# Performance work log

Hardware: AMD Instinct MI355X
Metric: run time of the kernel (lower is better)

## Reference

```python
import jax, jax.numpy as jnp
import numpy as np

B, T, D, F, E = 8, 2048, 1024, 4096, 16
C_FACTOR = 1.25
LB_W = 0.01


def setup_inputs() -> dict:
    key = jax.random.key(0)
    ks = jax.random.split(key, 4)
    x = jax.random.normal(ks[0], (B, T, D), dtype=jnp.float32)
    Wr = jax.random.normal(ks[1], (E, D), dtype=jnp.float32) * 0.02
    W1 = jax.random.normal(ks[2], (E, F, D), dtype=jnp.float32) * 0.02
    b1 = jnp.zeros((E, F), dtype=jnp.float32)
    W2 = jax.random.normal(ks[3], (E, D, F), dtype=jnp.float32) * 0.02
    b2 = jnp.zeros((E, D), dtype=jnp.float32)
    return {"x": x, "Wr": Wr, "W1": W1, "b1": b1, "W2": W2, "b2": b2}


def reference(x, Wr, W1, b1, W2, b2):
    Bs, Ts, Ds = x.shape
    Es = Wr.shape[0]
    tokens = Bs * Ts
    xf = x.reshape(tokens, Ds)

    # router
    logits = xf @ Wr.T                       # [tokens, E]
    probs = jax.nn.softmax(logits, axis=-1)
    top1 = jnp.argmax(probs, axis=-1)        # [tokens]
    top1p = jnp.max(probs, axis=-1)          # [tokens]

    capacity = int(C_FACTOR * tokens / Es)   # static python int

    onehot = jax.nn.one_hot(top1, Es, dtype=jnp.int32)        # [tokens, E]
    f = onehot.sum(axis=0).astype(probs.dtype) / tokens
    p = probs.mean(axis=0)
    lb_loss = Es * jnp.sum(f * p) * LB_W

    # faithful reproduction of idx[::expert_capacity]: among tokens routed to
    # expert e (in token order), keep only those whose rank % capacity == 0
    ranks = jnp.cumsum(onehot, axis=0) - 1                     # [tokens, E]
    keep = (onehot == 1) & (ranks % capacity == 0)             # [tokens, E]
    K = (tokens - 1) // capacity + 1                           # static max kept per expert

    idx = jax.vmap(lambda m: jnp.nonzero(m, size=K, fill_value=0)[0])(keep.T)  # [E, K]
    valid = jnp.take_along_axis(keep.T, idx, axis=1)           # [E, K] bool

    xg = xf[idx]                                               # [E, K, D]
    h = jax.nn.gelu(jnp.einsum('ekd,efd->ekf', xg, W1) + b1[:, None, :], approximate=False)
    eo = jnp.einsum('ekf,edf->ekd', h, W2) + b2[:, None, :]    # [E, K, D]
    scale = top1p[idx] * valid.astype(eo.dtype)                # [E, K]
    eo = eo * scale[..., None]

    out = jnp.zeros_like(xf).at[idx.reshape(-1)].add(eo.reshape(-1, Ds))
    return out.reshape(Bs, Ts, Ds), lb_loss
```

## Files before the change

kernel.cpp:

```cpp
#include <hip/hip_runtime.h>
#include <math.h>


#define TOKENS 16384
#define DD     1024
#define FF     4096
#define EE     16
#define CAP    1280
#define KMAX   13
#define NBLK   256

__global__ __launch_bounds__(256) void router_kernel(
    const float* __restrict__ x, const float* __restrict__ Wr,
    int* __restrict__ top1, float* __restrict__ top1p,
    int* __restrict__ blockhist, float* __restrict__ blockpsum)
{
    __shared__ float wrj[EE * 256];
    __shared__ float p_acc[EE];
    __shared__ int   hist[EE];

    const int tid  = threadIdx.x;
    const int wave = tid >> 6;
    const int lane = tid & 63;
    const int blk  = blockIdx.x;

    if (tid < EE) { p_acc[tid] = 0.0f; hist[tid] = 0; }

    for (int it = 0; it < 4; ++it) {
        const int tbase = blk * 64 + wave * 16 + it * 4;

        float4 xr[4][4];
        #pragma unroll
        for (int t = 0; t < 4; ++t) {
            const float4* xp = (const float4*)(x + (size_t)(tbase + t) * DD);
            #pragma unroll
            for (int j = 0; j < 4; ++j) xr[t][j] = xp[j * 64 + lane];
        }

        float acc[4][EE];
        #pragma unroll
        for (int t = 0; t < 4; ++t)
            #pragma unroll
            for (int e = 0; e < EE; ++e) acc[t][e] = 0.0f;

        for (int j = 0; j < 4; ++j) {
            __syncthreads();
            #pragma unroll
            for (int k = 0; k < 4; ++k) {
                int i = tid + k * 256;
                int e = i >> 6, c = i & 63;
                ((float4*)wrj)[i] = ((const float4*)Wr)[e * 256 + j * 64 + c];
            }
            __syncthreads();
            #pragma unroll
            for (int e = 0; e < EE; ++e) {
                float4 w = ((const float4*)(wrj + e * 256))[lane];
                #pragma unroll
                for (int t = 0; t < 4; ++t) {
                    acc[t][e] += xr[t][j].x * w.x + xr[t][j].y * w.y
                               + xr[t][j].z * w.z + xr[t][j].w * w.w;
                }
            }
        }

        #pragma unroll
        for (int t = 0; t < 4; ++t)
            #pragma unroll
            for (int e = 0; e < EE; ++e) {
                float v = acc[t][e];
                v += __shfl_xor(v, 32);
                v += __shfl_xor(v, 16);
                v += __shfl_xor(v, 8);
                v += __shfl_xor(v, 4);
                v += __shfl_xor(v, 2);
                v += __shfl_xor(v, 1);
                acc[t][e] = v;
            }

        if (lane < 4) {
            float lg[EE];
            #pragma unroll
            for (int e = 0; e < EE; ++e) {
                float v = acc[3][e];
                if (lane == 2) v = acc[2][e];
                if (lane == 1) v = acc[1][e];
                if (lane == 0) v = acc[0][e];
                lg[e] = v;
            }
            const int gt = tbase + lane;
            float mx = lg[0]; int bi = 0;
            #pragma unroll
            for (int e = 1; e < EE; ++e)
                if (lg[e] > mx) { mx = lg[e]; bi = e; }
            float pr[EE];
            float s = 0.0f;
            #pragma unroll
            for (int e = 0; e < EE; ++e) { pr[e] = expf(lg[e] - mx); s += pr[e]; }
            const float inv = 1.0f / s;
            top1[gt]  = bi;
            top1p[gt] = inv;
            #pragma unroll
            for (int e = 0; e < EE; ++e) atomicAdd(&p_acc[e], pr[e] * inv);
            atomicAdd(&hist[bi], 1);
        }
    }
    __syncthreads();
    if (tid < EE) {
        blockhist[blk * EE + tid] = hist[tid];
        blockpsum[blk * EE + tid] = p_acc[tid];
    }
}

__global__ __launch_bounds__(256) void scan_kernel(
    const int* __restrict__ blockhist, const float* __restrict__ blockpsum,
    int* __restrict__ base, int* __restrict__ nkept,
    const int* __restrict__ top1, float* __restrict__ mult0,
    float* __restrict__ lb_out)
{
    __shared__ int   hist_l[NBLK * EE];
    __shared__ int   gsum[EE * 16];
    __shared__ float fps[EE * 16];
    __shared__ float fp[EE];
    __shared__ int   nk_l[EE];

    const int tid = threadIdx.x;
    for (int i = tid; i < NBLK * EE; i += 256) hist_l[i] = blockhist[i];
    __syncthreads();

    const int e = tid >> 4, g = tid & 15;
    int s = 0;
    float sp = 0.0f;
    for (int b = g * 16; b < g * 16 + 16; ++b) {
        s  += hist_l[b * EE + e];
        sp += blockpsum[b * EE + e];
    }
    gsum[e * 16 + g] = s;
    fps[e * 16 + g]  = sp;
    __syncthreads();

    int pre = 0;
    for (int g2 = 0; g2 < g; ++g2) pre += gsum[e * 16 + g2];
    int run = pre;
    for (int b = g * 16; b < g * 16 + 16; ++b) {
        base[b * EE + e] = run;
        run += hist_l[b * EE + e];
    }
    if (g == 15) {
        const int c = run;
        const int nk = (c > 0) ? ((c - 1) / CAP + 1) : 0;
        nkept[e] = nk;
        nk_l[e]  = nk;
        float ps = 0.0f;
        for (int g2 = 0; g2 < 16; ++g2) ps += fps[e * 16 + g2];
        fp[e] = ((float)c / (float)TOKENS) * (ps / (float)TOKENS);
    }
    __syncthreads();
    if (tid == 0) {
        const int e0 = top1[0];
        mult0[0] = (float)(1 + KMAX - nk_l[e0]);
        float sum = 0.0f;
        for (int i = 0; i < EE; ++i) sum += fp[i];
        lb_out[0] = (float)EE * sum * 0.01f;
    }
}

__global__ __launch_bounds__(64) void keep_kernel(
    const int* __restrict__ top1, const float* __restrict__ top1p,
    const int* __restrict__ base, const float* __restrict__ mult0,
    int* __restrict__ kept_tok, float* __restrict__ kept_scale,
    int* __restrict__ slotmap)
{
    __shared__ int t1[64];
    const int tid = threadIdx.x;
    const int blk = blockIdx.x;
    const int gt  = blk * 64 + tid;
    const int e   = top1[gt];
    t1[tid] = e;
    __syncthreads();
    int r = 0;
    for (int i = 0; i < tid; ++i) r += (t1[i] == e) ? 1 : 0;
    const int rank = base[blk * EE + e] + r;
    int sm = -1;
    if (rank % CAP == 0) {
        const int slot = rank / CAP;
        sm = e * KMAX + slot;
        kept_tok[sm] = gt;
        float sc = top1p[gt];
        if (gt == 0) sc *= mult0[0];
        kept_scale[sm] = sc;
    }
    slotmap[gt] = sm;
}

__global__ __launch_bounds__(256) void expert1_kernel(
    const float* __restrict__ x, const float* __restrict__ W1,
    const float* __restrict__ b1, const int* __restrict__ nkept,
    const int* __restrict__ kept_tok, float* __restrict__ h)
{
    const int e    = blockIdx.x >> 8;
    const int fblk = blockIdx.x & 255;
    const int ne   = nkept[e];
    if (ne == 0) return;
    const int wave = threadIdx.x >> 6;
    const int lane = threadIdx.x & 63;

    for (int s = 0; s < ne; ++s) {
        const int t = kept_tok[e * KMAX + s];
        const float4* xp = (const float4*)(x + (size_t)t * DD);
        #pragma unroll
        for (int i = 0; i < 4; ++i) {
            const int f = fblk * 16 + wave * 4 + i;
            const float4* wrow = (const float4*)(W1 + ((size_t)e * FF + f) * DD);
            float d = 0.0f;
            #pragma unroll
            for (int k = 0; k < 4; ++k) {
                const float4 w  = wrow[k * 64 + lane];
                const float4 xv = xp[k * 64 + lane];
                d += w.x*xv.x + w.y*xv.y + w.z*xv.z + w.w*xv.w;
            }
            d += __shfl_xor(d, 32);
            d += __shfl_xor(d, 16);
            d += __shfl_xor(d, 8);
            d += __shfl_xor(d, 4);
            d += __shfl_xor(d, 2);
            d += __shfl_xor(d, 1);
            if (lane == 0) {
                const float v = d + b1[e * FF + f];
                h[((size_t)e * KMAX + s) * FF + f] =
                    0.5f * v * (1.0f + erff(v * 0.70710678118654752440f));
            }
        }
    }
}

__global__ __launch_bounds__(256) void expert2_kernel(
    const float* __restrict__ h, const float* __restrict__ W2,
    const float* __restrict__ b2, const int* __restrict__ nkept,
    const float* __restrict__ kept_scale, float* __restrict__ eo)
{
    const int e    = blockIdx.x >> 8;
    const int dblk = blockIdx.x & 255;
    const int ne   = nkept[e];
    if (ne == 0) return;
    const int wave = threadIdx.x >> 6;
    const int lane = threadIdx.x & 63;
    const int d    = dblk * 4 + wave;

    const float4* wrow = (const float4*)(W2 + ((size_t)e * DD + d) * FF);
    for (int s = 0; s < ne; ++s) {
        const float4* hp = (const float4*)(h + ((size_t)e * KMAX + s) * FF);
        float acc = 0.0f;
        #pragma unroll
        for (int k = 0; k < 16; ++k) {
            const float4 w  = wrow[k * 64 + lane];
            const float4 hv = hp[k * 64 + lane];
            acc += w.x*hv.x + w.y*hv.y + w.z*hv.z + w.w*hv.w;
        }
        acc += __shfl_xor(acc, 32);
        acc += __shfl_xor(acc, 16);
        acc += __shfl_xor(acc, 8);
        acc += __shfl_xor(acc, 4);
        acc += __shfl_xor(acc, 2);
        acc += __shfl_xor(acc, 1);
        if (lane == 0) {
            const float sc = kept_scale[e * KMAX + s];
            eo[((size_t)e * KMAX + s) * DD + d] = sc * (acc + b2[e * DD + d]);
        }
    }
}

__global__ __launch_bounds__(256) void expand_kernel(
    const float* __restrict__ eo, const int* __restrict__ slotmap,
    float* __restrict__ out)
{
    const int nf4 = TOKENS * DD / 4;
    int idx = blockIdx.x * 256 + threadIdx.x;
    const int stride = 4096 * 256;
    for (; idx < nf4; idx += stride) {
        const int t    = idx >> 8;
        const int slot = slotmap[t];
        float4 v = make_float4(0.0f, 0.0f, 0.0f, 0.0f);
        if (slot >= 0) v = ((const float4*)eo)[slot * 256 + (idx & 255)];
        ((float4*)out)[idx] = v;
    }
}

extern "C" void kernel_launch(void* const* d_in, const int* in_sizes, int n_in,
                              void* d_out, int out_size, void* d_ws, size_t ws_size,
                              hipStream_t stream) {
    const float* x  = (const float*)d_in[0];
    const float* Wr = (const float*)d_in[1];
    const float* W1 = (const float*)d_in[2];
    const float* b1 = (const float*)d_in[3];
    const float* W2 = (const float*)d_in[4];
    const float* b2 = (const float*)d_in[5];
    float* out = (float*)d_out;

    char* p = (char*)d_ws;
    int*   top1       = (int*)p;    p += (size_t)TOKENS * 4;
    float* top1p      = (float*)p;  p += (size_t)TOKENS * 4;
    int*   slotmap    = (int*)p;    p += (size_t)TOKENS * 4;
    int*   blockhist  = (int*)p;    p += (size_t)NBLK * EE * 4;
    float* blockpsum  = (float*)p;  p += (size_t)NBLK * EE * 4;
    int*   base       = (int*)p;    p += (size_t)NBLK * EE * 4;
    int*   nkept      = (int*)p;    p += 256;
    float* mult0      = (float*)p;  p += 256;
    int*   kept_tok   = (int*)p;    p += 1024;
    float* kept_scale = (float*)p;  p += 1024;
    float* eo         = (float*)p;  p += (size_t)EE * KMAX * DD * 4;
    float* h          = (float*)p;  p += (size_t)EE * KMAX * FF * 4;
    (void)ws_size; (void)in_sizes; (void)n_in;

    router_kernel<<<NBLK, 256, 0, stream>>>(x, Wr, top1, top1p,
                                            blockhist, blockpsum);
    scan_kernel<<<1, 256, 0, stream>>>(blockhist, blockpsum, base, nkept,
                                       top1, mult0, out + (size_t)out_size - 1);
    keep_kernel<<<NBLK, 64, 0, stream>>>(top1, top1p, base, mult0,
                                         kept_tok, kept_scale, slotmap);
    expert1_kernel<<<EE * 256, 256, 0, stream>>>(x, W1, b1, nkept, kept_tok, h);
    expert2_kernel<<<EE * 256, 256, 0, stream>>>(h, W2, b2, nkept, kept_scale, eo);
    expand_kernel<<<4096, 256, 0, stream>>>(eo, slotmap, out);
}
```

Measured before the change: 667.9 us.

## Retile router, expert GEMV, and scan kernels for more parallelism and reuse

The router now uses twice as many blocks, each covering 32 tokens, and reads Wr straight from global/L1 instead of staging it through LDS with barriers. The scan and keep kernels change to match the 32-token histogram granularity. expert1 issues all W1 and x loads up front and writes h as a float4. expert2 caches the h row in LDS and computes two output rows per wave. Together these aim to raise memory-level parallelism and cut sync overhead, at the cost of more registers and a finer-grained scan.

```diff
diff --git a/kernel.cpp b/kernel.cpp
--- a/kernel.cpp
+++ b/kernel.cpp
@@ -8,14 +8,13 @@
 #define EE     16
 #define CAP    1280
 #define KMAX   13
-#define NBLK   256
+#define NBLK   512
 
 __global__ __launch_bounds__(256) void router_kernel(
     const float* __restrict__ x, const float* __restrict__ Wr,
     int* __restrict__ top1, float* __restrict__ top1p,
     int* __restrict__ blockhist, float* __restrict__ blockpsum)
 {
-    __shared__ float wrj[EE * 256];
     __shared__ float p_acc[EE];
     __shared__ int   hist[EE];
 
@@ -25,17 +24,15 @@
     const int blk  = blockIdx.x;
 
     if (tid < EE) { p_acc[tid] = 0.0f; hist[tid] = 0; }
-
-    for (int it = 0; it < 4; ++it) {
-        const int tbase = blk * 64 + wave * 16 + it * 4;
-
-        float4 xr[4][4];
-        #pragma unroll
-        for (int t = 0; t < 4; ++t) {
-            const float4* xp = (const float4*)(x + (size_t)(tbase + t) * DD);
-            #pragma unroll
-            for (int j = 0; j < 4; ++j) xr[t][j] = xp[j * 64 + lane];
-        }
+    __syncthreads();
+
+    const float4* Wr4 = (const float4*)Wr;
+    for (int it = 0; it < 2; ++it) {
+        const int tbase = blk * 32 + wave * 8 + it * 4;
+        const float4* xp0 = (const float4*)(x + (size_t)(tbase + 0) * DD);
+        const float4* xp1 = (const float4*)(x + (size_t)(tbase + 1) * DD);
+        const float4* xp2 = (const float4*)(x + (size_t)(tbase + 2) * DD);
+        const float4* xp3 = (const float4*)(x + (size_t)(tbase + 3) * DD);
 
         float acc[4][EE];
         #pragma unroll
@@ -43,23 +40,19 @@
             #pragma unroll
             for (int e = 0; e < EE; ++e) acc[t][e] = 0.0f;
 
+        #pragma unroll
         for (int j = 0; j < 4; ++j) {
-            __syncthreads();
-            #pragma unroll
-            for (int k = 0; k < 4; ++k) {
-                int i = tid + k * 256;
-                int e = i >> 6, c = i & 63;
-                ((float4*)wrj)[i] = ((const float4*)Wr)[e * 256 + j * 64 + c];
-            }
-            __syncthreads();
+            const float4 x0 = xp0[j * 64 + lane];
+            const float4 x1 = xp1[j * 64 + lane];
+            const float4 x2 = xp2[j * 64 + lane];
+            const float4 x3 = xp3[j * 64 + lane];
             #pragma unroll
             for (int e = 0; e < EE; ++e) {
-                float4 w = ((const float4*)(wrj + e * 256))[lane];
-                #pragma unroll
-                for (int t = 0; t < 4; ++t) {
-                    acc[t][e] += xr[t][j].x * w.x + xr[t][j].y * w.y
-                               + xr[t][j].z * w.z + xr[t][j].w * w.w;
-                }
+                const float4 w = Wr4[e * 256 + j * 64 + lane];
+                acc[0][e] += x0.x*w.x + x0.y*w.y + x0.z*w.z + x0.w*w.w;
+                acc[1][e] += x1.x*w.x + x1.y*w.y + x1.z*w.z + x1.w*w.w;
+                acc[2][e] += x2.x*w.x + x2.y*w.y + x2.z*w.z + x2.w*w.w;
+                acc[3][e] += x3.x*w.x + x3.y*w.y + x3.z*w.z + x3.w*w.w;
             }
         }
 
@@ -130,7 +123,7 @@
     const int e = tid >> 4, g = tid & 15;
     int s = 0;
     float sp = 0.0f;
-    for (int b = g * 16; b < g * 16 + 16; ++b) {
+    for (int b = g * 32; b < g * 32 + 32; ++b) {
         s  += hist_l[b * EE + e];
         sp += blockpsum[b * EE + e];
     }
@@ -141,7 +134,7 @@
     int pre = 0;
     for (int g2 = 0; g2 < g; ++g2) pre += gsum[e * 16 + g2];
     int run = pre;
-    for (int b = g * 16; b < g * 16 + 16; ++b) {
+    for (int b = g * 32; b < g * 32 + 32; ++b) {
         base[b * EE + e] = run;
         run += hist_l[b * EE + e];
     }
@@ -177,9 +170,11 @@
     const int e   = top1[gt];
     t1[tid] = e;
     __syncthreads();
+    const int start = tid & 32;
     int r = 0;
-    for (int i = 0; i < tid; ++i) r += (t1[i] == e) ? 1 : 0;
-    const int rank = base[blk * EE + e] + r;
+    for (int i = start; i < tid; ++i) r += (t1[i] == e) ? 1 : 0;
+    const int hb   = gt >> 5;
+    const int rank = base[hb * EE + e] + r;
     int sm = -1;
     if (rank % CAP == 0) {
         const int slot = rank / CAP;
@@ -203,32 +198,61 @@
     if (ne == 0) return;
     const int wave = threadIdx.x >> 6;
     const int lane = threadIdx.x & 63;
+    const int f0   = fblk * 16 + wave * 4;
+    const float4* wr0 = (const float4*)(W1 + ((size_t)e * FF + f0) * DD);
 
     for (int s = 0; s < ne; ++s) {
         const int t = kept_tok[e * KMAX + s];
         const float4* xp = (const float4*)(x + (size_t)t * DD);
+        float4 xv[4];
+        #pragma unroll
+        for (int k = 0; k < 4; ++k) xv[k] = xp[k * 64 + lane];
+
+        float4 wv[4][4];
+        #pragma unroll
+        for (int i = 0; i < 4; ++i)
+            #pragma unroll
+            for (int k = 0; k < 4; ++k)
+                wv[i][k] = wr0[i * 256 + k * 64 + lane];
+
+        float d[4];
         #pragma unroll
         for (int i = 0; i < 4; ++i) {
-            const int f = fblk * 16 + wave * 4 + i;
-            const float4* wrow = (const float4*)(W1 + ((size_t)e * FF + f) * DD);
-            float d = 0.0f;
+            float acc = 0.0f;
             #pragma unroll
             for (int k = 0; k < 4; ++k) {
-                const float4 w  = wrow[k * 64 + lane];
-                const float4 xv = xp[k * 64 + lane];
-                d += w.x*xv.x + w.y*xv.y + w.z*xv.z + w.w*xv.w;
-            }
-            d += __shfl_xor(d, 32);
-            d += __shfl_xor(d, 16);
-            d += __shfl_xor(d, 8);
-            d += __shfl_xor(d, 4);
-            d += __shfl_xor(d, 2);
-            d += __shfl_xor(d, 1);
-            if (lane == 0) {
-                const float v = d + b1[e * FF + f];
-                h[((size_t)e * KMAX + s) * FF + f] =
-                    0.5f * v * (1.0f + erff(v * 0.70710678118654752440f));
-            }
+                acc += wv[i][k].x * xv[k].x + wv[i][k].y * xv[k].y
+                     + wv[i][k].z * xv[k].z + wv[i][k].w * xv[k].w;
+            }
+            d[i] = acc;
+        }
+
+        #pragma unroll
+        for (int off = 32; off >= 1; off >>= 1) {
+            #pragma unroll
+            for (int i = 0; i < 4; ++i) d[i] += __shfl_xor(d[i], off);
+        }
+
+        if (lane == 0) {
+            const float* bp = b1 + e * FF + f0;
+            float4 hv;
+            {
+                const float v = d[0] + bp[0];
+                hv.x = 0.5f * v * (1.0f + erff(v * 0.70710678118654752440f));
+            }
+            {
+                const float v = d[1] + bp[1];
+                hv.y = 0.5f * v * (1.0f + erff(v * 0.70710678118654752440f));
+            }
+            {
+                const float v = d[2] + bp[2];
+                hv.z = 0.5f * v * (1.0f + erff(v * 0.70710678118654752440f));
+            }
+            {
+                const float v = d[3] + bp[3];
+                hv.w = 0.5f * v * (1.0f + erff(v * 0.70710678118654752440f));
+            }
+            *(float4*)(h + ((size_t)e * KMAX + s) * FF + f0) = hv;
         }
     }
 }
@@ -238,33 +262,44 @@
     const float* __restrict__ b2, const int* __restrict__ nkept,
     const float* __restrict__ kept_scale, float* __restrict__ eo)
 {
-    const int e    = blockIdx.x >> 8;
-    const int dblk = blockIdx.x & 255;
+    __shared__ float hs[FF];
+    const int e    = blockIdx.x >> 7;
+    const int dblk = blockIdx.x & 127;
     const int ne   = nkept[e];
     if (ne == 0) return;
-    const int wave = threadIdx.x >> 6;
-    const int lane = threadIdx.x & 63;
-    const int d    = dblk * 4 + wave;
-
-    const float4* wrow = (const float4*)(W2 + ((size_t)e * DD + d) * FF);
+    const int tid  = threadIdx.x;
+    const int wave = tid >> 6;
+    const int lane = tid & 63;
+    const int d0   = dblk * 8 + wave * 2;
+
+    const float4* wr0 = (const float4*)(W2 + ((size_t)e * DD + d0) * FF);
     for (int s = 0; s < ne; ++s) {
+        __syncthreads();
         const float4* hp = (const float4*)(h + ((size_t)e * KMAX + s) * FF);
-        float acc = 0.0f;
+        #pragma unroll
+        for (int q = 0; q < 4; ++q)
+            ((float4*)hs)[q * 256 + tid] = hp[q * 256 + tid];
+        __syncthreads();
+
+        float a0 = 0.0f, a1 = 0.0f;
         #pragma unroll
         for (int k = 0; k < 16; ++k) {
-            const float4 w  = wrow[k * 64 + lane];
-            const float4 hv = hp[k * 64 + lane];
-            acc += w.x*hv.x + w.y*hv.y + w.z*hv.z + w.w*hv.w;
-        }
-        acc += __shfl_xor(acc, 32);
-        acc += __shfl_xor(acc, 16);
-        acc += __shfl_xor(acc, 8);
-        acc += __shfl_xor(acc, 4);
-        acc += __shfl_xor(acc, 2);
-        acc += __shfl_xor(acc, 1);
+            const float4 w0 = wr0[k * 64 + lane];
+            const float4 w1 = wr0[1024 + k * 64 + lane];
+            const float4 hv = ((const float4*)hs)[k * 64 + lane];
+            a0 += w0.x*hv.x + w0.y*hv.y + w0.z*hv.z + w0.w*hv.w;
+            a1 += w1.x*hv.x + w1.y*hv.y + w1.z*hv.z + w1.w*hv.w;
+        }
+        #pragma unroll
+        for (int off = 32; off >= 1; off >>= 1) {
+            a0 += __shfl_xor(a0, off);
+            a1 += __shfl_xor(a1, off);
+        }
         if (lane == 0) {
             const float sc = kept_scale[e * KMAX + s];
-            eo[((size_t)e * KMAX + s) * DD + d] = sc * (acc + b2[e * DD + d]);
+            float* ep = eo + ((size_t)e * KMAX + s) * DD + d0;
+            ep[0] = sc * (a0 + b2[e * DD + d0]);
+            ep[1] = sc * (a1 + b2[e * DD + d0 + 1]);
         }
     }
 }
@@ -315,9 +350,9 @@
                                             blockhist, blockpsum);
     scan_kernel<<<1, 256, 0, stream>>>(blockhist, blockpsum, base, nkept,
                                        top1, mult0, out + (size_t)out_size - 1);
-    keep_kernel<<<NBLK, 64, 0, stream>>>(top1, top1p, base, mult0,
-                                         kept_tok, kept_scale, slotmap);
+    keep_kernel<<<256, 64, 0, stream>>>(top1, top1p, base, mult0,
+                                        kept_tok, kept_scale, slotmap);
     expert1_kernel<<<EE * 256, 256, 0, stream>>>(x, W1, b1, nkept, kept_tok, h);
-    expert2_kernel<<<EE * 256, 256, 0, stream>>>(h, W2, b2, nkept, kept_scale, eo);
+    expert2_kernel<<<EE * 128, 256, 0, stream>>>(h, W2, b2, nkept, kept_scale, eo);
     expand_kernel<<<4096, 256, 0, stream>>>(eo, slotmap, out);
 }
```

Result: slower. 689.8 us (+3.3%).
